# Kernel tuning notes

Measured on AMD Instinct MI355X. Metric: run time of the kernel, lower is better.

The kernel has to match this reference:

```python
import jax, jax.numpy as jnp
import numpy as np

C, H, W = 4, 512, 512  # featuremap: (C, feature_width, feature_height) -> (C, H_in, W_in)
HID = 16
N = 4_000_000


def _lin_init(key, fan_in, fan_out):
    kw, kb = jax.random.split(key)
    bound = 1.0 / np.sqrt(fan_in)
    Wm = jax.random.uniform(kw, (fan_in, fan_out), jnp.float32, -bound, bound)
    b = jax.random.uniform(kb, (fan_out,), jnp.float32, -bound, bound)
    return Wm, b


def setup_inputs() -> dict:
    key = jax.random.key(0)
    ks = jax.random.split(key, 7)
    x = jax.random.uniform(ks[0], (N, 3), jnp.float32)
    featuremap = 0.1 * jax.random.normal(ks[1], (C, H, W), jnp.float32)
    W1, b1 = _lin_init(ks[2], 7, HID)
    W2, b2 = _lin_init(ks[3], HID, HID)
    W3, b3 = _lin_init(ks[4], HID, HID)
    W4, b4 = _lin_init(ks[5], HID, HID)
    W5, b5 = _lin_init(ks[6], HID, 3)
    return {"x": x, "featuremap": featuremap, "W1": W1, "b1": b1, "W2": W2,
            "b2": b2, "W3": W3, "b3": b3, "W4": W4, "b4": b4, "W5": W5, "b5": b5}


def _grid_sample_border(fm, uv):
    # fm: [C, H_in, W_in]; uv: [N, 2] in [0,1], col0 -> width (x), col1 -> height (y)
    # matches F.grid_sample(mode='bilinear', padding_mode='border', align_corners=False)
    c, h, w = fm.shape
    g = uv * 2.0 - 1.0
    fx = jnp.clip(((g[:, 0] + 1.0) * w - 1.0) * 0.5, 0.0, w - 1.0)
    fy = jnp.clip(((g[:, 1] + 1.0) * h - 1.0) * 0.5, 0.0, h - 1.0)
    x0 = jnp.floor(fx)
    y0 = jnp.floor(fy)
    wx1 = fx - x0
    wy1 = fy - y0
    ix0 = x0.astype(jnp.int32)
    iy0 = y0.astype(jnp.int32)
    ix1 = jnp.minimum(ix0 + 1, w - 1)
    iy1 = jnp.minimum(iy0 + 1, h - 1)
    v00 = fm[:, iy0, ix0]  # [C, N]
    v01 = fm[:, iy0, ix1]
    v10 = fm[:, iy1, ix0]
    v11 = fm[:, iy1, ix1]
    out = (v00 * ((1.0 - wy1) * (1.0 - wx1)) + v01 * ((1.0 - wy1) * wx1)
           + v10 * (wy1 * (1.0 - wx1)) + v11 * (wy1 * wx1))
    return out.T  # [N, C]


def reference(x, featuremap, W1, b1, W2, b2, W3, b3, W4, b4, W5, b5):
    feat = _grid_sample_border(featuremap, x[:, :2])  # [N, 4]
    h = jnp.concatenate([x, feat], axis=-1)           # [N, 7]
    h = jax.nn.relu(h @ W1 + b1)
    h = jax.nn.relu(h @ W2 + b2)
    h = jax.nn.relu(h @ W3 + b3)
    h = jax.nn.relu(h @ W4 + b4)
    return h @ W5 + b5
```

## Files before the change

kernel.cpp:

```cpp
#include <hip/hip_runtime.h>

#define HH 512
#define WW 512
#define HWSZ (HH * WW)
#define BLK 256
#define TPB 8

#define SW1 20
#define O_W1 0
#define O_B1 140
#define O_W2 156
#define O_B2 476
#define O_W3 492
#define O_B3 812
#define O_W4 828
#define O_B4 1148
#define O_W5 1164
#define O_B5 1228
#define SWF_TOT 1244

typedef __fp16 f16x2 __attribute__((ext_vector_type(2)));
typedef __fp16 f16x4 __attribute__((ext_vector_type(4)));
typedef float f32x4 __attribute__((ext_vector_type(4)));

#define MFMA16(a, b, c) __builtin_amdgcn_mfma_f32_16x16x16f16((a), (b), (c), 0, 0, 0)

__device__ inline unsigned pk2u(float a, float b) {
    f16x2 p;
    p[0] = (__fp16)a;
    p[1] = (__fp16)b;
    return __builtin_bit_cast(unsigned, p);
}

__device__ inline f16x4 relu_pack(f32x4 d) {
    f16x4 r;
    r[0] = (__fp16)fmaxf(d[0], 0.f);
    r[1] = (__fp16)fmaxf(d[1], 0.f);
    r[2] = (__fp16)fmaxf(d[2], 0.f);
    r[3] = (__fp16)fmaxf(d[3], 0.f);
    return r;
}

__global__ void fm_transpose_h(const float* __restrict__ fm, f16x4* __restrict__ fmT) {
    int i = blockIdx.x * blockDim.x + threadIdx.x;
    if (i < HWSZ) {
        f16x4 v;
        v[0] = (__fp16)fm[i];
        v[1] = (__fp16)fm[HWSZ + i];
        v[2] = (__fp16)fm[2 * HWSZ + i];
        v[3] = (__fp16)fm[3 * HWSZ + i];
        fmT[i] = v;
    }
}

template <bool TR>
__global__ __launch_bounds__(BLK) void mlp_fused(
    const float* __restrict__ x, const void* __restrict__ fmv,
    const float* __restrict__ W1, const float* __restrict__ b1,
    const float* __restrict__ W2, const float* __restrict__ b2,
    const float* __restrict__ W3, const float* __restrict__ b3,
    const float* __restrict__ W4, const float* __restrict__ b4,
    const float* __restrict__ W5, const float* __restrict__ b5,
    float* __restrict__ out, int n)
{
    __shared__ __align__(16) float sW[SWF_TOT];
    __shared__ __align__(16) unsigned sX[2][BLK * 4];
    const int tid = threadIdx.x;

    if (tid < 112) { int r = tid >> 4, c = tid & 15; sW[O_W1 + r * SW1 + c] = W1[tid]; }
    if (tid < 16) {
        sW[O_B1 + tid] = b1[tid];
        sW[O_B2 + tid] = b2[tid];
        sW[O_B3 + tid] = b3[tid];
        sW[O_B4 + tid] = b4[tid];
        sW[O_B5 + tid] = (tid < 3) ? b5[tid] : 0.f;
    }
    {
        int r = tid >> 4, c = tid & 15;
        sW[O_W2 + r * SW1 + c] = W2[tid];
        sW[O_W3 + r * SW1 + c] = W3[tid];
        sW[O_W4 + r * SW1 + c] = W4[tid];
    }
    if (tid < 48) { int r = tid / 3, c = tid % 3; sW[O_W5 + r * 4 + c] = W5[tid]; }

    const int lane = tid & 63;
    const int wv = tid >> 6;
    const int jj = lane & 15;
    const int kg = lane >> 4;
    const int tile0 = blockIdx.x * TPB;

    const f16x4* fmH = reinterpret_cast<const f16x4*>(fmv);
    const float* fmf = reinterpret_cast<const float*>(fmv);

    float pa0, pa1, pa2;
    float pb0, pb1, pb2;
    uint2 gv00, gv01, gv10, gv11;

    auto loadX = [&](int t, float& q0, float& q1, float& q2) {
        int p = (tile0 + t) * BLK + tid;
        int ii = (p < n) ? p : (n - 1);
        q0 = x[3 * ii]; q1 = x[3 * ii + 1]; q2 = x[3 * ii + 2];
    };
    auto addr = [&](float q0, float q1, int& ix0, int& iy0, int& ix1, int& iy1,
                    float& wxo, float& wyo) {
        float gx = q0 * 2.f - 1.f;
        float gy = q1 * 2.f - 1.f;
        float fx = ((gx + 1.f) * (float)WW - 1.f) * 0.5f;
        float fy = ((gy + 1.f) * (float)HH - 1.f) * 0.5f;
        fx = fminf(fmaxf(fx, 0.f), (float)(WW - 1));
        fy = fminf(fmaxf(fy, 0.f), (float)(HH - 1));
        float x0f = floorf(fx), y0f = floorf(fy);
        wxo = fx - x0f; wyo = fy - y0f;
        ix0 = (int)x0f; iy0 = (int)y0f;
        ix1 = min(ix0 + 1, WW - 1);
        iy1 = min(iy0 + 1, HH - 1);
    };
    auto issueG = [&](float q0, float q1) {
        if (TR) {
            int ix0, iy0, ix1, iy1; float wxo, wyo;
            addr(q0, q1, ix0, iy0, ix1, iy1, wxo, wyo);
            const uint2* f2 = reinterpret_cast<const uint2*>(fmH);
            gv00 = f2[iy0 * WW + ix0];
            gv01 = f2[iy0 * WW + ix1];
            gv10 = f2[iy1 * WW + ix0];
            gv11 = f2[iy1 * WW + ix1];
        }
    };
    auto interpPackWrite = [&](float q0, float q1, float q2, int buf) {
        int ix0, iy0, ix1, iy1; float wxo, wyo;
        addr(q0, q1, ix0, iy0, ix1, iy1, wxo, wyo);
        float w00 = (1.f - wyo) * (1.f - wxo);
        float w01 = (1.f - wyo) * wxo;
        float w10 = wyo * (1.f - wxo);
        float w11 = wyo * wxo;
        float feat[4];
        if (TR) {
            f16x4 v00 = __builtin_bit_cast(f16x4, gv00);
            f16x4 v01 = __builtin_bit_cast(f16x4, gv01);
            f16x4 v10 = __builtin_bit_cast(f16x4, gv10);
            f16x4 v11 = __builtin_bit_cast(f16x4, gv11);
#pragma unroll
            for (int ch = 0; ch < 4; ++ch) {
                feat[ch] = (float)v00[ch] * w00 + (float)v01[ch] * w01 +
                           (float)v10[ch] * w10 + (float)v11[ch] * w11;
            }
        } else {
#pragma unroll
            for (int ch = 0; ch < 4; ++ch) {
                const float* f = fmf + ch * HWSZ;
                feat[ch] = f[iy0 * WW + ix0] * w00 + f[iy0 * WW + ix1] * w01 +
                           f[iy1 * WW + ix0] * w10 + f[iy1 * WW + ix1] * w11;
            }
        }
        uint4 rec;
        rec.x = pk2u(q0, q1);
        rec.y = pk2u(q2, feat[0]);
        rec.z = pk2u(feat[1], feat[2]);
        rec.w = pk2u(feat[3], 0.f);
        reinterpret_cast<uint4*>(sX[buf])[tid] = rec;
    };

    f16x4 A1, A2, A3, A4, A5;
    f32x4 C1, C2, C3, C4, C5;

    auto runTile = [&](int t, int buf) {
        const unsigned* sxb = sX[buf];
        f16x4 B0, B1f, B2f, B3f;
        const int pb = wv * 64;
#define LOADB(Bv, g)                                                         \
        {                                                                    \
            uint2 raw = make_uint2(0u, 0u);                                  \
            if (kg < 2)                                                      \
                raw = *reinterpret_cast<const uint2*>(                       \
                    sxb + (pb + (g) * 16 + jj) * 4 + kg * 2);                \
            (Bv) = __builtin_bit_cast(f16x4, raw);                           \
        }
        LOADB(B0, 0) LOADB(B1f, 1) LOADB(B2f, 2) LOADB(B3f, 3)
#undef LOADB
        f32x4 D0, D1, D2, D3;
        D0 = MFMA16(A1, B0, C1);  D1 = MFMA16(A1, B1f, C1);
        D2 = MFMA16(A1, B2f, C1); D3 = MFMA16(A1, B3f, C1);
        B0 = relu_pack(D0); B1f = relu_pack(D1); B2f = relu_pack(D2); B3f = relu_pack(D3);
        D0 = MFMA16(A2, B0, C2);  D1 = MFMA16(A2, B1f, C2);
        D2 = MFMA16(A2, B2f, C2); D3 = MFMA16(A2, B3f, C2);
        B0 = relu_pack(D0); B1f = relu_pack(D1); B2f = relu_pack(D2); B3f = relu_pack(D3);
        D0 = MFMA16(A3, B0, C3);  D1 = MFMA16(A3, B1f, C3);
        D2 = MFMA16(A3, B2f, C3); D3 = MFMA16(A3, B3f, C3);
        B0 = relu_pack(D0); B1f = relu_pack(D1); B2f = relu_pack(D2); B3f = relu_pack(D3);
        D0 = MFMA16(A4, B0, C4);  D1 = MFMA16(A4, B1f, C4);
        D2 = MFMA16(A4, B2f, C4); D3 = MFMA16(A4, B3f, C4);
        B0 = relu_pack(D0); B1f = relu_pack(D1); B2f = relu_pack(D2); B3f = relu_pack(D3);
        D0 = MFMA16(A5, B0, C5);  D1 = MFMA16(A5, B1f, C5);
        D2 = MFMA16(A5, B2f, C5); D3 = MFMA16(A5, B3f, C5);
        if (kg == 0) {
            const int gbase = (tile0 + t) * BLK + wv * 64 + jj;
#define STOREG(Dv, g)                                                        \
            {                                                                \
                int gp = gbase + (g) * 16;                                   \
                if (gp < n) {                                                \
                    out[3 * gp]     = (Dv)[0];                               \
                    out[3 * gp + 1] = (Dv)[1];                               \
                    out[3 * gp + 2] = (Dv)[2];                               \
                }                                                            \
            }
            STOREG(D0, 0) STOREG(D1, 1) STOREG(D2, 2) STOREG(D3, 3)
#undef STOREG
        }
    };

    {
        float q0, q1, q2;
        loadX(0, q0, q1, q2);
        issueG(q0, q1);
        interpPackWrite(q0, q1, q2, 0);
    }
    loadX(1, pa0, pa1, pa2);
    __syncthreads();

#pragma unroll
    for (int e = 0; e < 4; ++e) {
        int k = 4 * kg + e;
        A1[e] = (__fp16)((k < 7) ? sW[O_W1 + k * SW1 + jj] : 0.f);
        A2[e] = (__fp16)sW[O_W2 + k * SW1 + jj];
        A3[e] = (__fp16)sW[O_W3 + k * SW1 + jj];
        A4[e] = (__fp16)sW[O_W4 + k * SW1 + jj];
        A5[e] = (__fp16)((jj < 3) ? sW[O_W5 + k * 4 + jj] : 0.f);
    }
    C1 = *reinterpret_cast<const f32x4*>(sW + O_B1 + 4 * kg);
    C2 = *reinterpret_cast<const f32x4*>(sW + O_B2 + 4 * kg);
    C3 = *reinterpret_cast<const f32x4*>(sW + O_B3 + 4 * kg);
    C4 = *reinterpret_cast<const f32x4*>(sW + O_B4 + 4 * kg);
    C5 = *reinterpret_cast<const f32x4*>(sW + O_B5 + 4 * kg);

    issueG(pa0, pa1);

#pragma unroll 1
    for (int t = 0; t < TPB; ++t) {
        const int cur = t & 1;
        if (t + 2 < TPB) loadX(t + 2, pb0, pb1, pb2);
        runTile(t, cur);
        if (t + 1 < TPB) interpPackWrite(pa0, pa1, pa2, cur ^ 1);
        pa0 = pb0; pa1 = pb1; pa2 = pb2;
        __syncthreads();
        if (t + 2 < TPB) issueG(pa0, pa1);
    }
}

extern "C" void kernel_launch(void* const* d_in, const int* in_sizes, int n_in,
                              void* d_out, int out_size, void* d_ws, size_t ws_size,
                              hipStream_t stream) {
    const float* x  = (const float*)d_in[0];
    const float* fm = (const float*)d_in[1];
    const float* W1 = (const float*)d_in[2];
    const float* b1 = (const float*)d_in[3];
    const float* W2 = (const float*)d_in[4];
    const float* b2 = (const float*)d_in[5];
    const float* W3 = (const float*)d_in[6];
    const float* b3 = (const float*)d_in[7];
    const float* W4 = (const float*)d_in[8];
    const float* b4 = (const float*)d_in[9];
    const float* W5 = (const float*)d_in[10];
    const float* b5 = (const float*)d_in[11];
    float* out = (float*)d_out;

    const int n = in_sizes[0] / 3;
    const int tiles = (n + BLK - 1) / BLK;
    const int grid = (tiles + TPB - 1) / TPB;

    const size_t need = (size_t)HWSZ * sizeof(f16x4);
    if (ws_size >= need) {
        f16x4* fmT = (f16x4*)d_ws;
        fm_transpose_h<<<(HWSZ + 255) / 256, 256, 0, stream>>>(fm, fmT);
        mlp_fused<true><<<grid, BLK, 0, stream>>>(x, (const void*)fmT, W1, b1,
                                                  W2, b2, W3, b3, W4, b4, W5, b5,
                                                  out, n);
    } else {
        mlp_fused<false><<<grid, BLK, 0, stream>>>(x, (const void*)fm, W1, b1,
                                                   W2, b2, W3, b3, W4, b4, W5, b5,
                                                   out, n);
    }
}
```

Measured before the change: 166.5 us.

## Interpolate features in packed fp16 and halve tiles per block

Bilinear interpolation now runs in packed half precision on fp16 feature vectors. The sample weights are computed once at gather issue instead of recomputing the address math. The input record layout is rearranged so the four features occupy a whole 64-bit slot, with a zero row inserted into W1 to match. ReLU-pack uses packed conversion plus a vector max, and TPB drops from 8 to 4, which doubles the number of blocks. The changes cut ALU work and raise parallelism, at the cost of fp16 rounding in the interpolation and more per-block weight-setup overhead.

```diff
diff --git a/kernel.cpp b/kernel.cpp
--- a/kernel.cpp
+++ b/kernel.cpp
@@ -4,23 +4,24 @@
 #define WW 512
 #define HWSZ (HH * WW)
 #define BLK 256
-#define TPB 8
+#define TPB 4
 
 #define SW1 20
 #define O_W1 0
-#define O_B1 140
-#define O_W2 156
-#define O_B2 476
-#define O_W3 492
-#define O_B3 812
-#define O_W4 828
-#define O_B4 1148
-#define O_W5 1164
-#define O_B5 1228
-#define SWF_TOT 1244
+#define O_W2 160
+#define O_W3 480
+#define O_W4 800
+#define O_W5 1120
+#define O_B1 1184
+#define O_B2 1200
+#define O_B3 1216
+#define O_B4 1232
+#define O_B5 1248
+#define SWF_TOT 1264
 
 typedef __fp16 f16x2 __attribute__((ext_vector_type(2)));
 typedef __fp16 f16x4 __attribute__((ext_vector_type(4)));
+typedef _Float16 h16x4 __attribute__((ext_vector_type(4)));
 typedef float f32x4 __attribute__((ext_vector_type(4)));
 
 #define MFMA16(a, b, c) __builtin_amdgcn_mfma_f32_16x16x16f16((a), (b), (c), 0, 0, 0)
@@ -33,12 +34,14 @@
 }
 
 __device__ inline f16x4 relu_pack(f32x4 d) {
-    f16x4 r;
-    r[0] = (__fp16)fmaxf(d[0], 0.f);
-    r[1] = (__fp16)fmaxf(d[1], 0.f);
-    r[2] = (__fp16)fmaxf(d[2], 0.f);
-    r[3] = (__fp16)fmaxf(d[3], 0.f);
-    return r;
+    f16x2 lo = __builtin_amdgcn_cvt_pkrtz(d[0], d[1]);
+    f16x2 hi = __builtin_amdgcn_cvt_pkrtz(d[2], d[3]);
+    uint2 u = make_uint2(__builtin_bit_cast(unsigned, lo),
+                         __builtin_bit_cast(unsigned, hi));
+    h16x4 r = __builtin_bit_cast(h16x4, u);
+    h16x4 z = {};
+    r = __builtin_elementwise_max(r, z);
+    return __builtin_bit_cast(f16x4, r);
 }
 
 __global__ void fm_transpose_h(const float* __restrict__ fm, f16x4* __restrict__ fmT) {
@@ -67,7 +70,12 @@
     __shared__ __align__(16) unsigned sX[2][BLK * 4];
     const int tid = threadIdx.x;
 
-    if (tid < 112) { int r = tid >> 4, c = tid & 15; sW[O_W1 + r * SW1 + c] = W1[tid]; }
+    if (tid < 112) {
+        int r = tid >> 4, c = tid & 15;
+        int rr = (r < 3) ? r : r + 1;
+        sW[O_W1 + rr * SW1 + c] = W1[tid];
+    }
+    if (tid >= 112 && tid < 132) sW[O_W1 + 3 * SW1 + (tid - 112)] = 0.f;
     if (tid < 16) {
         sW[O_B1 + tid] = b1[tid];
         sW[O_B2 + tid] = b2[tid];
@@ -89,12 +97,11 @@
     const int kg = lane >> 4;
     const int tile0 = blockIdx.x * TPB;
 
-    const f16x4* fmH = reinterpret_cast<const f16x4*>(fmv);
     const float* fmf = reinterpret_cast<const float*>(fmv);
 
-    float pa0, pa1, pa2;
-    float pb0, pb1, pb2;
+    float pa0, pa1, pa2, pb0, pb1, pb2;
     uint2 gv00, gv01, gv10, gv11;
+    float wxs, wys;
 
     auto loadX = [&](int t, float& q0, float& q1, float& q2) {
         int p = (tile0 + t) * BLK + tid;
@@ -117,9 +124,9 @@
     };
     auto issueG = [&](float q0, float q1) {
         if (TR) {
-            int ix0, iy0, ix1, iy1; float wxo, wyo;
-            addr(q0, q1, ix0, iy0, ix1, iy1, wxo, wyo);
-            const uint2* f2 = reinterpret_cast<const uint2*>(fmH);
+            int ix0, iy0, ix1, iy1;
+            addr(q0, q1, ix0, iy0, ix1, iy1, wxs, wys);
+            const uint2* f2 = reinterpret_cast<const uint2*>(fmv);
             gv00 = f2[iy0 * WW + ix0];
             gv01 = f2[iy0 * WW + ix1];
             gv10 = f2[iy1 * WW + ix0];
@@ -127,36 +134,44 @@
         }
     };
     auto interpPackWrite = [&](float q0, float q1, float q2, int buf) {
-        int ix0, iy0, ix1, iy1; float wxo, wyo;
-        addr(q0, q1, ix0, iy0, ix1, iy1, wxo, wyo);
-        float w00 = (1.f - wyo) * (1.f - wxo);
-        float w01 = (1.f - wyo) * wxo;
-        float w10 = wyo * (1.f - wxo);
-        float w11 = wyo * wxo;
-        float feat[4];
+        uint2 fz;
         if (TR) {
-            f16x4 v00 = __builtin_bit_cast(f16x4, gv00);
-            f16x4 v01 = __builtin_bit_cast(f16x4, gv01);
-            f16x4 v10 = __builtin_bit_cast(f16x4, gv10);
-            f16x4 v11 = __builtin_bit_cast(f16x4, gv11);
-#pragma unroll
-            for (int ch = 0; ch < 4; ++ch) {
-                feat[ch] = (float)v00[ch] * w00 + (float)v01[ch] * w01 +
-                           (float)v10[ch] * w10 + (float)v11[ch] * w11;
-            }
+            float w00 = (1.f - wys) * (1.f - wxs);
+            float w01 = (1.f - wys) * wxs;
+            float w10 = wys * (1.f - wxs);
+            float w11 = wys * wxs;
+            _Float16 h00 = (_Float16)w00, h01 = (_Float16)w01;
+            _Float16 h10 = (_Float16)w10, h11 = (_Float16)w11;
+            h16x4 W00 = {h00, h00, h00, h00}, W01 = {h01, h01, h01, h01};
+            h16x4 W10 = {h10, h10, h10, h10}, W11 = {h11, h11, h11, h11};
+            h16x4 v00 = __builtin_bit_cast(h16x4, gv00);
+            h16x4 v01 = __builtin_bit_cast(h16x4, gv01);
+            h16x4 v10 = __builtin_bit_cast(h16x4, gv10);
+            h16x4 v11 = __builtin_bit_cast(h16x4, gv11);
+            h16x4 acc = v00 * W00 + v01 * W01 + v10 * W10 + v11 * W11;
+            fz = __builtin_bit_cast(uint2, acc);
         } else {
+            int ix0, iy0, ix1, iy1; float wxo, wyo;
+            addr(q0, q1, ix0, iy0, ix1, iy1, wxo, wyo);
+            float w00 = (1.f - wyo) * (1.f - wxo);
+            float w01 = (1.f - wyo) * wxo;
+            float w10 = wyo * (1.f - wxo);
+            float w11 = wyo * wxo;
+            float feat[4];
 #pragma unroll
             for (int ch = 0; ch < 4; ++ch) {
                 const float* f = fmf + ch * HWSZ;
                 feat[ch] = f[iy0 * WW + ix0] * w00 + f[iy0 * WW + ix1] * w01 +
                            f[iy1 * WW + ix0] * w10 + f[iy1 * WW + ix1] * w11;
             }
+            fz.x = pk2u(feat[0], feat[1]);
+            fz.y = pk2u(feat[2], feat[3]);
         }
         uint4 rec;
         rec.x = pk2u(q0, q1);
-        rec.y = pk2u(q2, feat[0]);
-        rec.z = pk2u(feat[1], feat[2]);
-        rec.w = pk2u(feat[3], 0.f);
+        rec.y = pk2u(q2, 0.f);
+        rec.z = fz.x;
+        rec.w = fz.y;
         reinterpret_cast<uint4*>(sX[buf])[tid] = rec;
     };
 
@@ -220,7 +235,7 @@
 #pragma unroll
     for (int e = 0; e < 4; ++e) {
         int k = 4 * kg + e;
-        A1[e] = (__fp16)((k < 7) ? sW[O_W1 + k * SW1 + jj] : 0.f);
+        A1[e] = (__fp16)((k < 8) ? sW[O_W1 + k * SW1 + jj] : 0.f);
         A2[e] = (__fp16)sW[O_W2 + k * SW1 + jj];
         A3[e] = (__fp16)sW[O_W3 + k * SW1 + jj];
         A4[e] = (__fp16)sW[O_W4 + k * SW1 + jj];
```

Measured after the change: 164.1 us. About the same (-1.4%).
